# Optimization experiments

Measured on AMD Instinct MI355X. Metric: run time of the kernel, lower is better.

The kernel has to match this reference:

```python
import jax, jax.numpy as jnp
import numpy as np

B, S, IN, H, D, OUT = 4, 4096, 1024, 16, 64, 1024


def setup_inputs() -> dict:
    key = jax.random.key(0)
    k1, k2, k3, k4, k5 = jax.random.split(key, 5)
    x = jax.random.normal(k1, (B, S, IN), dtype=jnp.float32)
    input_state = jnp.zeros((B, H, D), dtype=jnp.float32)
    # parameters
    w_in = jax.random.normal(k2, (H * D, IN), dtype=jnp.float32) * (1.0 / np.sqrt(IN))
    state_weight = jax.random.normal(k3, (H, D, D), dtype=jnp.float32) * (1.0 / np.sqrt(D))
    state_bias = jax.random.normal(k4, (H, D), dtype=jnp.float32) * 0.02
    w_out = jax.random.normal(k5, (OUT, H * D), dtype=jnp.float32) * (1.0 / np.sqrt(H * D))
    return {"x": x, "input_state": input_state, "w_in": w_in,
            "state_weight": state_weight, "state_bias": state_bias, "w_out": w_out}


def reference(x, input_state, w_in, state_weight, state_bias, w_out):
    # input projection: [B, S, IN] -> [B, S, H, D]
    xp = jnp.einsum('bsi,ki->bsk', x, w_in).reshape(B, S, H, D)
    xs = jnp.transpose(xp, (1, 0, 2, 3))  # [S, B, H, D] for scan over time

    def step(h, x_t):
        # h: [B, H, D]; per-head recurrence h_t = tanh(W_h h_{t-1} + b + x_t)
        h_new = jnp.tanh(jnp.einsum('hed,bhd->bhe', state_weight, h)
                         + state_bias[None] + x_t)
        return h_new, h_new

    _, ys = jax.lax.scan(step, input_state, xs)  # ys: [S, B, H, D]
    y = jnp.transpose(ys, (1, 0, 2, 3)).reshape(B, S, H * D)
    return jnp.einsum('bsk,ok->bso', y, w_out)
```

## Files before the change

### kernel.cpp

```cpp
#include <hip/hip_runtime.h>

#define B_ 4
#define S_ 4096
#define IN_ 1024
#define H_ 16
#define D_ 64
#define OUT_ 1024
#define HD_ 1024
#define M_ 16384

typedef __bf16 bf16x8 __attribute__((ext_vector_type(8)));
typedef __bf16 bf16x2 __attribute__((ext_vector_type(2)));
typedef float floatx4 __attribute__((ext_vector_type(4)));

static __device__ __forceinline__ unsigned int f2bf(float f) {
    unsigned int u = __builtin_bit_cast(unsigned int, f);
    u += 0x7fffu + ((u >> 16) & 1u);
    return u >> 16;
}

static __device__ __forceinline__ float dot2bf(unsigned int a, unsigned int b, float c) {
    return __builtin_amdgcn_fdot2_f32_bf16(__builtin_bit_cast(bf16x2, a),
                                           __builtin_bit_cast(bf16x2, b), c, false);
}

__global__ void cast_f32_bf16(const float* __restrict__ src,
                              unsigned short* __restrict__ dst, int n4) {
    int i = blockIdx.x * blockDim.x + threadIdx.x;
    if (i < n4) {
        float4 v = ((const float4*)src)[i];
        ushort4 o;
        o.x = (unsigned short)f2bf(v.x); o.y = (unsigned short)f2bf(v.y);
        o.z = (unsigned short)f2bf(v.z); o.w = (unsigned short)f2bf(v.w);
        ((ushort4*)dst)[i] = o;
    }
}

#define LSTR 40
__global__ __launch_bounds__(256) void gemm_bt(
    const unsigned short* __restrict__ A,
    const unsigned short* __restrict__ Bm,
    float* __restrict__ C, int M, int N, int K) {
    __shared__ unsigned short As[128 * LSTR];
    __shared__ unsigned short Bs[128 * LSTR];
    const int t = threadIdx.x;
    const int lane = t & 63;
    const int wave = t >> 6;
    const int wm = wave >> 1, wn = wave & 1;
    const int m0 = blockIdx.y * 128;
    const int n0 = blockIdx.x * 128;
    const int l16 = lane & 15;
    const int quad = lane >> 4;

    floatx4 acc[4][4];
#pragma unroll
    for (int i = 0; i < 4; i++)
#pragma unroll
        for (int j = 0; j < 4; j++) acc[i][j] = (floatx4){0.f, 0.f, 0.f, 0.f};

    for (int k0 = 0; k0 < K; k0 += 32) {
#pragma unroll
        for (int it = 0; it < 2; it++) {
            int c = it * 256 + t;
            int row = c >> 2;
            int kc = c & 3;
            uint4 va = *(const uint4*)(A + (size_t)(m0 + row) * K + k0 + kc * 8);
            *(uint4*)(As + row * LSTR + kc * 8) = va;
            uint4 vb = *(const uint4*)(Bm + (size_t)(n0 + row) * K + k0 + kc * 8);
            *(uint4*)(Bs + row * LSTR + kc * 8) = vb;
        }
        __syncthreads();
        bf16x8 af[4], bfr[4];
#pragma unroll
        for (int i = 0; i < 4; i++)
            af[i] = *(const bf16x8*)(As + (wm * 64 + i * 16 + l16) * LSTR + quad * 8);
#pragma unroll
        for (int j = 0; j < 4; j++)
            bfr[j] = *(const bf16x8*)(Bs + (wn * 64 + j * 16 + l16) * LSTR + quad * 8);
#pragma unroll
        for (int i = 0; i < 4; i++)
#pragma unroll
            for (int j = 0; j < 4; j++)
                acc[i][j] = __builtin_amdgcn_mfma_f32_16x16x32_bf16(
                    af[i], bfr[j], acc[i][j], 0, 0, 0);
        __syncthreads();
    }
#pragma unroll
    for (int i = 0; i < 4; i++)
#pragma unroll
        for (int j = 0; j < 4; j++)
#pragma unroll
            for (int r = 0; r < 4; r++) {
                int row = m0 + wm * 64 + i * 16 + quad * 4 + r;
                int col = n0 + wn * 64 + j * 16 + l16;
                C[(size_t)row * N + col] = acc[i][j][r];
            }
}

__global__ __launch_bounds__(64, 1) void rnn_scan(
    const float* __restrict__ xp,
    const float* __restrict__ w_h,
    const float* __restrict__ bias,
    const float* __restrict__ h0,
    unsigned short* __restrict__ y) {
    const int bh = blockIdx.x;
    const int b = bh >> 4;
    const int h = bh & 15;
    const int e = threadIdx.x;

    unsigned int W2[32];
    const float* wrow = w_h + ((size_t)(h * 64 + e)) * 64;
#pragma unroll
    for (int j = 0; j < 16; j++) {
        float4 v = ((const float4*)wrow)[j];
        W2[2 * j]     = f2bf(v.x) | (f2bf(v.y) << 16);
        W2[2 * j + 1] = f2bf(v.z) | (f2bf(v.w) << 16);
    }
    const float be = bias[h * 64 + e];
    unsigned int hb = f2bf(h0[(b * 16 + h) * 64 + e]);

    const float* xb = xp + ((size_t)(b * S_) * 16 + h) * 64 + e;
    unsigned short* yb = y + ((size_t)(b * S_) * 16 + h) * 64 + e;

    float xA[8], xB[8];
#pragma unroll
    for (int i2 = 0; i2 < 8; i2++) xA[i2] = xb[(size_t)i2 * 1024];
#pragma unroll
    for (int i2 = 0; i2 < 8; i2++) xB[i2] = xb[(size_t)(8 + i2) * 1024];

    auto step = [&](int t, float xv) {
        unsigned int hbs = (unsigned int)__builtin_amdgcn_update_dpp(
            0, (int)hb, 0xF5, 0xF, 0xF, true);
        unsigned int pk = (hbs << 16) | hb;
        float a0 = 0.f, a1 = 0.f, a2 = 0.f, a3 = 0.f;
#pragma unroll
        for (int k = 0; k < 8; k++) {
            unsigned int s0 = (unsigned int)__builtin_amdgcn_readlane((int)pk, 8 * k + 0);
            unsigned int s1 = (unsigned int)__builtin_amdgcn_readlane((int)pk, 8 * k + 2);
            unsigned int s2 = (unsigned int)__builtin_amdgcn_readlane((int)pk, 8 * k + 4);
            unsigned int s3 = (unsigned int)__builtin_amdgcn_readlane((int)pk, 8 * k + 6);
            a0 = dot2bf(s0, W2[4 * k + 0], a0);
            a1 = dot2bf(s1, W2[4 * k + 1], a1);
            a2 = dot2bf(s2, W2[4 * k + 2], a2);
            a3 = dot2bf(s3, W2[4 * k + 3], a3);
        }
        float sum = (a0 + a1) + (a2 + a3);
        float pre = sum + (be + xv);
        float em = __builtin_amdgcn_exp2f(fabsf(pre) * -2.885390081777927f);
        float rr = (1.0f - em) * __builtin_amdgcn_rcpf(1.0f + em);
        float hn = copysignf(rr, pre);
        hb = f2bf(hn);
        yb[(size_t)t * 1024] = (unsigned short)hb;
    };

    for (int t0 = 0; t0 < S_; t0 += 16) {
#pragma unroll
        for (int u = 0; u < 8; u++) step(t0 + u, xA[u]);
        if (t0 + 16 < S_) {
#pragma unroll
            for (int i2 = 0; i2 < 8; i2++) xA[i2] = xb[(size_t)(t0 + 16 + i2) * 1024];
        }
#pragma unroll
        for (int u = 0; u < 8; u++) step(t0 + 8 + u, xB[u]);
        if (t0 + 24 < S_) {
#pragma unroll
            for (int i2 = 0; i2 < 8; i2++) xB[i2] = xb[(size_t)(t0 + 24 + i2) * 1024];
        }
    }
}

extern "C" void kernel_launch(void* const* d_in, const int* in_sizes, int n_in,
                              void* d_out, int out_size, void* d_ws, size_t ws_size,
                              hipStream_t stream) {
    const float* x     = (const float*)d_in[0];
    const float* h0    = (const float*)d_in[1];
    const float* w_in  = (const float*)d_in[2];
    const float* w_h   = (const float*)d_in[3];
    const float* bias  = (const float*)d_in[4];
    const float* w_out = (const float*)d_in[5];
    float* out = (float*)d_out;

    char* ws = (char*)d_ws;
    unsigned short* x_bf    = (unsigned short*)(ws);
    unsigned short* win_bf  = (unsigned short*)(ws + (size_t)33554432);
    unsigned short* wout_bf = (unsigned short*)(ws + (size_t)35651584);
    unsigned short* y_bf    = (unsigned short*)(ws + (size_t)37748736);

    {
        int n4 = (M_ * IN_) / 4;
        cast_f32_bf16<<<(n4 + 255) / 256, 256, 0, stream>>>(x, x_bf, n4);
        int w4 = (HD_ * IN_) / 4;
        cast_f32_bf16<<<(w4 + 255) / 256, 256, 0, stream>>>(w_in, win_bf, w4);
        cast_f32_bf16<<<(w4 + 255) / 256, 256, 0, stream>>>(w_out, wout_bf, w4);
    }
    dim3 g1(HD_ / 128, M_ / 128);
    gemm_bt<<<g1, 256, 0, stream>>>(x_bf, win_bf, out, M_, HD_, IN_);
    rnn_scan<<<64, 64, 0, stream>>>(out, w_h, bias, h0, y_bf);
    dim3 g2(OUT_ / 128, M_ / 128);
    gemm_bt<<<g2, 256, 0, stream>>>(y_bf, wout_bf, out, M_, OUT_, HD_);
}
```

Measured before the change: 981.8 us.

## Compute per-step RNN matvec with MFMA using bpermute-broadcast hidden state

Replaces the per-step readlane plus fdot2 matrix-vector product in the recurrent scan with eight 16x16x32 bf16 MFMA instructions. The hidden state is broadcast into A fragments via ds_bpermute, the weights are preloaded as B fragments in registers, and the result column is gathered back with more bpermutes and selects. This aims to shorten the serial per-timestep latency chain, at the cost of MFMA latency, LDS-crossbar permutes, and wasted MFMA rows, since only one row of each tile is useful.

```diff
diff --git a/kernel.cpp b/kernel.cpp
--- a/kernel.cpp
+++ b/kernel.cpp
@@ -12,16 +12,12 @@
 typedef __bf16 bf16x8 __attribute__((ext_vector_type(8)));
 typedef __bf16 bf16x2 __attribute__((ext_vector_type(2)));
 typedef float floatx4 __attribute__((ext_vector_type(4)));
+typedef int int32x4 __attribute__((ext_vector_type(4)));
 
 static __device__ __forceinline__ unsigned int f2bf(float f) {
     unsigned int u = __builtin_bit_cast(unsigned int, f);
     u += 0x7fffu + ((u >> 16) & 1u);
     return u >> 16;
-}
-
-static __device__ __forceinline__ float dot2bf(unsigned int a, unsigned int b, float c) {
-    return __builtin_amdgcn_fdot2_f32_bf16(__builtin_bit_cast(bf16x2, a),
-                                           __builtin_bit_cast(bf16x2, b), c, false);
 }
 
 __global__ void cast_f32_bf16(const float* __restrict__ src,
@@ -107,15 +103,34 @@
     const int b = bh >> 4;
     const int h = bh & 15;
     const int e = threadIdx.x;
-
-    unsigned int W2[32];
-    const float* wrow = w_h + ((size_t)(h * 64 + e)) * 64;
-#pragma unroll
-    for (int j = 0; j < 16; j++) {
-        float4 v = ((const float4*)wrow)[j];
-        W2[2 * j]     = f2bf(v.x) | (f2bf(v.y) << 16);
-        W2[2 * j + 1] = f2bf(v.z) | (f2bf(v.w) << 16);
-    }
+    const int c = e & 15;
+    const int q = e >> 4;
+    const int q8 = q * 8;
+
+    auto loadB = [&](int nt, int kt) -> bf16x8 {
+        const float* wr = w_h + ((size_t)(h * 64 + nt * 16 + c)) * 64 + kt * 32 + q8;
+        float4 v0 = ((const float4*)wr)[0];
+        float4 v1 = ((const float4*)wr)[1];
+        int32x4 bi;
+        bi[0] = (int)(f2bf(v0.x) | (f2bf(v0.y) << 16));
+        bi[1] = (int)(f2bf(v0.z) | (f2bf(v0.w) << 16));
+        bi[2] = (int)(f2bf(v1.x) | (f2bf(v1.y) << 16));
+        bi[3] = (int)(f2bf(v1.z) | (f2bf(v1.w) << 16));
+        return __builtin_bit_cast(bf16x8, bi);
+    };
+    const bf16x8 Bf00 = loadB(0, 0), Bf01 = loadB(0, 1);
+    const bf16x8 Bf10 = loadB(1, 0), Bf11 = loadB(1, 1);
+    const bf16x8 Bf20 = loadB(2, 0), Bf21 = loadB(2, 1);
+    const bf16x8 Bf30 = loadB(3, 0), Bf31 = loadB(3, 1);
+
+    const int aA00 = (q8 + 0) * 4, aA01 = (q8 + 2) * 4,
+              aA02 = (q8 + 4) * 4, aA03 = (q8 + 6) * 4;
+    const int aA10 = aA00 + 128, aA11 = aA01 + 128,
+              aA12 = aA02 + 128, aA13 = aA03 + 128;
+    const int aY = c * 4;
+    const bool oddq = (q & 1) != 0;
+    const bool hiq  = (q & 2) != 0;
+
     const float be = bias[h * 64 + e];
     unsigned int hb = f2bf(h0[(b * 16 + h) * 64 + e]);
 
@@ -131,21 +146,39 @@
     auto step = [&](int t, float xv) {
         unsigned int hbs = (unsigned int)__builtin_amdgcn_update_dpp(
             0, (int)hb, 0xF5, 0xF, 0xF, true);
-        unsigned int pk = (hbs << 16) | hb;
-        float a0 = 0.f, a1 = 0.f, a2 = 0.f, a3 = 0.f;
-#pragma unroll
-        for (int k = 0; k < 8; k++) {
-            unsigned int s0 = (unsigned int)__builtin_amdgcn_readlane((int)pk, 8 * k + 0);
-            unsigned int s1 = (unsigned int)__builtin_amdgcn_readlane((int)pk, 8 * k + 2);
-            unsigned int s2 = (unsigned int)__builtin_amdgcn_readlane((int)pk, 8 * k + 4);
-            unsigned int s3 = (unsigned int)__builtin_amdgcn_readlane((int)pk, 8 * k + 6);
-            a0 = dot2bf(s0, W2[4 * k + 0], a0);
-            a1 = dot2bf(s1, W2[4 * k + 1], a1);
-            a2 = dot2bf(s2, W2[4 * k + 2], a2);
-            a3 = dot2bf(s3, W2[4 * k + 3], a3);
-        }
-        float sum = (a0 + a1) + (a2 + a3);
-        float pre = sum + (be + xv);
+        int pk = (int)((hbs << 16) | hb);
+        int32x4 a0i, a1i;
+        a0i[0] = __builtin_amdgcn_ds_bpermute(aA00, pk);
+        a0i[1] = __builtin_amdgcn_ds_bpermute(aA01, pk);
+        a0i[2] = __builtin_amdgcn_ds_bpermute(aA02, pk);
+        a0i[3] = __builtin_amdgcn_ds_bpermute(aA03, pk);
+        a1i[0] = __builtin_amdgcn_ds_bpermute(aA10, pk);
+        a1i[1] = __builtin_amdgcn_ds_bpermute(aA11, pk);
+        a1i[2] = __builtin_amdgcn_ds_bpermute(aA12, pk);
+        a1i[3] = __builtin_amdgcn_ds_bpermute(aA13, pk);
+        bf16x8 A0 = __builtin_bit_cast(bf16x8, a0i);
+        bf16x8 A1 = __builtin_bit_cast(bf16x8, a1i);
+        const floatx4 z4 = (floatx4){0.f, 0.f, 0.f, 0.f};
+        floatx4 ac0 = __builtin_amdgcn_mfma_f32_16x16x32_bf16(A0, Bf00, z4, 0, 0, 0);
+        floatx4 ac1 = __builtin_amdgcn_mfma_f32_16x16x32_bf16(A0, Bf10, z4, 0, 0, 0);
+        floatx4 ac2 = __builtin_amdgcn_mfma_f32_16x16x32_bf16(A0, Bf20, z4, 0, 0, 0);
+        floatx4 ac3 = __builtin_amdgcn_mfma_f32_16x16x32_bf16(A0, Bf30, z4, 0, 0, 0);
+        ac0 = __builtin_amdgcn_mfma_f32_16x16x32_bf16(A1, Bf01, ac0, 0, 0, 0);
+        ac1 = __builtin_amdgcn_mfma_f32_16x16x32_bf16(A1, Bf11, ac1, 0, 0, 0);
+        ac2 = __builtin_amdgcn_mfma_f32_16x16x32_bf16(A1, Bf21, ac2, 0, 0, 0);
+        ac3 = __builtin_amdgcn_mfma_f32_16x16x32_bf16(A1, Bf31, ac3, 0, 0, 0);
+        float y0 = __builtin_bit_cast(float,
+            __builtin_amdgcn_ds_bpermute(aY, __builtin_bit_cast(int, ac0[0])));
+        float y1 = __builtin_bit_cast(float,
+            __builtin_amdgcn_ds_bpermute(aY, __builtin_bit_cast(int, ac1[0])));
+        float y2 = __builtin_bit_cast(float,
+            __builtin_amdgcn_ds_bpermute(aY, __builtin_bit_cast(int, ac2[0])));
+        float y3 = __builtin_bit_cast(float,
+            __builtin_amdgcn_ds_bpermute(aY, __builtin_bit_cast(int, ac3[0])));
+        float y01 = oddq ? y1 : y0;
+        float y23 = oddq ? y3 : y2;
+        float yv  = hiq ? y23 : y01;
+        float pre = yv + (be + xv);
         float em = __builtin_amdgcn_exp2f(fabsf(pre) * -2.885390081777927f);
         float rr = (1.0f - em) * __builtin_amdgcn_rcpf(1.0f + em);
         float hn = copysignf(rr, pre);
```

Result: slower. 1.182 ms (+20.4%).
